# Kernel optimization log

Measured on AMD Instinct MI355X. Metric: run time of the kernel, lower is better.

Reference implementation:

```python
import jax, jax.numpy as jnp
import numpy as np

B, N, IN_DIM, HID = 64, 1024, 128, 32


def _xavier(key, shape):
    # xavier_uniform_ on torch Linear weight [out, in]; we store [in, out]
    fan_in, fan_out = shape[0], shape[1]
    limit = float(np.sqrt(6.0 / (fan_in + fan_out)))
    return jax.random.uniform(key, shape, jnp.float32, -limit, limit)


def setup_inputs() -> dict:
    key = jax.random.key(0)
    ks = jax.random.split(key, 8)
    x = jax.random.normal(ks[0], (B, N, IN_DIM), jnp.float32)
    adj = jax.random.uniform(ks[1], (B, N, N), jnp.float32)  # dense adjacency
    W1 = _xavier(ks[2], (IN_DIM, HID))
    W2 = _xavier(ks[3], (HID, HID))
    W3 = _xavier(ks[4], (HID, HID))
    W4 = _xavier(ks[5], (HID, HID))
    b1 = jnp.zeros((HID,), jnp.float32)
    b2 = jnp.zeros((HID,), jnp.float32)
    b3 = jnp.zeros((HID,), jnp.float32)
    b4 = jnp.zeros((HID,), jnp.float32)
    a1 = jnp.float32(0.25)  # PReLU default init
    a2 = jnp.float32(0.25)
    a3 = jnp.float32(0.25)
    a4 = jnp.float32(0.25)
    return {"x": x, "adj": adj, "W1": W1, "W2": W2, "W3": W3, "W4": W4,
            "b1": b1, "b2": b2, "b3": b3, "b4": b4,
            "a1": a1, "a2": a2, "a3": a3, "a4": a4}


def _gcn_layer(x, adj, W, b, a):
    h = jnp.einsum('bnf,fo->bno', x, W)      # linear, no bias
    h = jnp.matmul(adj, h) + b               # aggregation + bias
    return jnp.where(h >= 0, h, a * h)       # PReLU


def reference(x, adj, W1, W2, W3, W4, b1, b2, b3, b4, a1, a2, a3, a4):
    h1 = _gcn_layer(x, adj, W1, b1, a1)
    h2 = _gcn_layer(h1, adj, W2, b2, a2)
    h3 = _gcn_layer(h2, adj, W3, b3, a3)
    h4 = _gcn_layer(h3, adj, W4, b4, a4)
    # sum-pool nodes per layer, concat along feature dim -> [B, 4*HID]
    return jnp.concatenate([h1.sum(axis=1), h2.sum(axis=1),
                            h3.sum(axis=1), h4.sum(axis=1)], axis=1)
```

## Files before the change

kernel.cpp:

```cpp
#include <hip/hip_runtime.h>
#include <hip/hip_bf16.h>

#define B_   64
#define N_   1024
#define IND_ 128
#define HID_ 32

typedef __attribute__((ext_vector_type(8))) short short8;
typedef __attribute__((ext_vector_type(4))) float f32x4;
typedef unsigned short u16;

static __device__ __forceinline__ u16 f2bf(float f) {
    union { __hip_bfloat16 h; u16 s; } u;
    u.h = __float2bfloat16(f);
    return u.s;
}
static __device__ __forceinline__ short8 cvt8(f32x4 v0, f32x4 v1) {
    union { short8 s; __hip_bfloat162 h[4]; } u;
    u.h[0] = __float22bfloat162_rn(float2{v0[0], v0[1]});
    u.h[1] = __float22bfloat162_rn(float2{v0[2], v0[3]});
    u.h[2] = __float22bfloat162_rn(float2{v1[0], v1[1]});
    u.h[3] = __float22bfloat162_rn(float2{v1[2], v1[3]});
    return u.s;
}

__global__ __launch_bounds__(256) void convert_tile_kernel(
    const float* __restrict__ adjf, u16* __restrict__ adjT)
{
    const int wslot = blockIdx.x * 4 + (threadIdx.x >> 6);
    const int lane = threadIdx.x & 63;
    const int r = lane & 15, g = lane >> 4;
    const int t0 = wslot * 16;
    const int b  = t0 >> 11;
    const int rt = (t0 >> 5) & 63;
    const int k0base = (t0 & 31) * 32;

    const float* src = adjf + ((size_t)b * N_ + rt * 16 + r) * N_ + k0base + g * 8;
    u16* dst = adjT + (size_t)t0 * 512 + lane * 8;
#pragma unroll 4
    for (int j = 0; j < 16; ++j) {
        f32x4 v0 = __builtin_nontemporal_load((const f32x4*)(src + j * 32));
        f32x4 v1 = __builtin_nontemporal_load((const f32x4*)(src + j * 32) + 1);
        *(short8*)(dst + (size_t)j * 512) = cvt8(v0, v1);
    }
}

template<int F>
__global__ __launch_bounds__(256) void linear_kernel(
    const float* __restrict__ in,
    const float* __restrict__ W,
    u16* __restrict__ hF)
{
    __shared__ float sW[F][HID_];
    const int tid = threadIdx.x;
    for (int e = tid; e < F * HID_; e += 256) sW[e / HID_][e % HID_] = W[e];
    __syncthreads();

    const int b = blockIdx.x >> 2;
    const int n = ((blockIdx.x & 3) << 8) + tid;
    const f32x4* row4 = (const f32x4*)(in + ((size_t)b * N_ + n) * F);

    float acc[HID_];
#pragma unroll
    for (int o = 0; o < HID_; ++o) acc[o] = 0.f;

#pragma unroll 4
    for (int f4 = 0; f4 < F / 4; ++f4) {
        f32x4 xv = __builtin_nontemporal_load(row4 + f4);
#pragma unroll
        for (int j = 0; j < 4; ++j)
#pragma unroll
            for (int o = 0; o < HID_; ++o) acc[o] += xv[j] * sW[f4 * 4 + j][o];
    }
    u16* op = hF + (size_t)b * (HID_ * N_) + (size_t)(n >> 5) * 1024
              + ((n >> 3) & 3) * 128 + (n & 7);
#pragma unroll
    for (int o = 0; o < HID_; ++o)
        op[(o >> 4) * 512 + (o & 15) * 8] = f2bf(acc[o]);
}

template<int MODE, int FUSE>
__global__ __launch_bounds__(256) void agg_kernel(
    const float* __restrict__ adjf,
    const u16*  __restrict__ adjT,
    const u16*  __restrict__ hF_in,
    u16*        __restrict__ hF_out,
    const float* __restrict__ Wnext,
    float*      __restrict__ h,
    float*      __restrict__ partial,
    const float* __restrict__ bias,
    const float* __restrict__ alpha_p)
{
    __shared__ float h_s[64][33];
    __shared__ float sW2[HID_][HID_];
    __shared__ float pool[4][HID_];

    const int tid = threadIdx.x;
    const int b = blockIdx.y;
    const int wid = tid >> 6, lane = tid & 63;
    const int r16 = lane & 15, g = lane >> 4;
    const int koff = g * 8;
    const int rowbase = blockIdx.x * 64 + wid * 16;
    const int row0 = rowbase + r16;

    if (FUSE) {
        for (int e = tid; e < HID_ * HID_; e += 256) ((float*)sW2)[e] = Wnext[e];
    }

    const u16* pbF = hF_in + (size_t)b * (HID_ * N_) + lane * 8;
    const u16* pa = (MODE == 0)
        ? adjT + ((size_t)b * 2048 + (size_t)(blockIdx.x * 4 + wid) * 32) * 512 + lane * 8
        : nullptr;
    const float* pf = (MODE == 2)
        ? adjf + ((size_t)b * N_ + row0) * N_ + koff
        : nullptr;

    f32x4 acc[2] = {};
#pragma unroll 8
    for (int ki = 0; ki < 32; ++ki) {
        short8 a0;
        if (MODE == 0) {
            a0 = *(const short8*)(pa + (size_t)ki * 512);
        } else {
            f32x4 v0 = __builtin_nontemporal_load((const f32x4*)(pf + ki * 32));
            f32x4 v1 = __builtin_nontemporal_load((const f32x4*)(pf + ki * 32) + 1);
            a0 = cvt8(v0, v1);
        }
        short8 b0 = *(const short8*)(pbF + (size_t)ki * 1024);
        short8 b1 = *(const short8*)(pbF + (size_t)ki * 1024 + 512);
        acc[0] = __builtin_amdgcn_mfma_f32_16x16x32_bf16(a0, b0, acc[0], 0, 0, 0);
        acc[1] = __builtin_amdgcn_mfma_f32_16x16x32_bf16(a0, b1, acc[1], 0, 0, 0);
    }

    const float alpha = *alpha_p;
    float v[2][4], ps[2];
#pragma unroll
    for (int ct = 0; ct < 2; ++ct) {
        const float bv = bias[ct * 16 + r16];
        ps[ct] = 0.f;
#pragma unroll
        for (int r = 0; r < 4; ++r) {
            float x = acc[ct][r] + bv;
            x = (x >= 0.f) ? x : alpha * x;
            v[ct][r] = x;
            ps[ct] += x;
        }
    }
#pragma unroll
    for (int ct = 0; ct < 2; ++ct) {
        const int col = ct * 16 + r16;
        float p = ps[ct];
        p += __shfl_xor(p, 16, 64);
        p += __shfl_xor(p, 32, 64);
        if (lane < 16) pool[wid][col] = p;
        if (FUSE) {
#pragma unroll
            for (int r = 0; r < 4; ++r)
                h_s[wid * 16 + g * 4 + r][col] = v[ct][r];
        }
        if (MODE == 2) {
#pragma unroll
            for (int r = 0; r < 4; ++r)
                h[((size_t)b * N_ + rowbase + g * 4 + r) * HID_ + col] = v[ct][r];
        }
    }
    __syncthreads();

    if (tid < HID_) {
        float s = pool[0][tid] + pool[1][tid] + pool[2][tid] + pool[3][tid];
        partial[((size_t)b * 16 + blockIdx.x) * HID_ + tid] = s;
    }

    if (FUSE) {
        const int r_local = tid >> 2;
        const int obase = (tid & 3) * 8;
        float acc2[8];
#pragma unroll
        for (int o = 0; o < 8; ++o) acc2[o] = 0.f;
#pragma unroll 4
        for (int k = 0; k < HID_; ++k) {
            const float hv = h_s[r_local][k];
#pragma unroll
            for (int o = 0; o < 8; ++o) acc2[o] += hv * sW2[k][obase + o];
        }
        const int n = blockIdx.x * 64 + r_local;
        u16* op = hF_out + (size_t)b * (HID_ * N_) + (size_t)(n >> 5) * 1024
                  + ((n >> 3) & 3) * 128 + (n & 7);
#pragma unroll
        for (int o = 0; o < 8; ++o) {
            const int oo = obase + o;
            op[(oo >> 4) * 512 + (oo & 15) * 8] = f2bf(acc2[o]);
        }
    }
}

__global__ __launch_bounds__(256) void finalize_kernel(
    const float* __restrict__ partial,
    float* __restrict__ out)
{
    const int i = blockIdx.x * 256 + threadIdx.x;
    if (i >= B_ * 4 * HID_) return;
    const int b = i >> 7;
    const int rem = i & 127;
    const int l = rem >> 5;
    const int o = rem & 31;
    const float* p = partial + (((size_t)l * B_ + b) * 16) * HID_ + o;
    float s = 0.f;
#pragma unroll
    for (int t = 0; t < 16; ++t) s += p[t * HID_];
    out[i] = s;
}

extern "C" void kernel_launch(void* const* d_in, const int* in_sizes, int n_in,
                              void* d_out, int out_size, void* d_ws, size_t ws_size,
                              hipStream_t stream) {
    const float* x   = (const float*)d_in[0];
    const float* adj = (const float*)d_in[1];
    const float* W[4]  = {(const float*)d_in[2], (const float*)d_in[3],
                          (const float*)d_in[4], (const float*)d_in[5]};
    const float* bi[4] = {(const float*)d_in[6], (const float*)d_in[7],
                          (const float*)d_in[8], (const float*)d_in[9]};
    const float* al[4] = {(const float*)d_in[10], (const float*)d_in[11],
                          (const float*)d_in[12], (const float*)d_in[13]};
    float* out = (float*)d_out;

    const size_t adjb_bytes = (size_t)B_ * N_ * N_ * 2;
    const size_t hlin_bytes = (size_t)B_ * HID_ * N_ * 2;
    const size_t h_bytes    = (size_t)B_ * N_ * HID_ * 4;
    const size_t part_bytes = (size_t)4 * B_ * 16 * HID_ * 4;
    const bool full = ws_size >= adjb_bytes + 2 * hlin_bytes + part_bytes;

    const dim3 ga(16, 64);
    const int part_stride = B_ * 16 * HID_;

    if (full) {
        char* p = (char*)d_ws;
        u16* adjT  = (u16*)p;  p += adjb_bytes;
        u16* hFA   = (u16*)p;  p += hlin_bytes;
        u16* hFB   = (u16*)p;  p += hlin_bytes;
        float* partial = (float*)p;

        convert_tile_kernel<<<2048, 256, 0, stream>>>(adj, adjT);
        linear_kernel<IND_><<<256, 256, 0, stream>>>(x, W[0], hFA);

        agg_kernel<0, 1><<<ga, 256, 0, stream>>>(nullptr, adjT, hFA, hFB,
                                                 W[1], nullptr,
                                                 partial + 0, bi[0], al[0]);
        agg_kernel<0, 1><<<ga, 256, 0, stream>>>(nullptr, adjT, hFB, hFA,
                                                 W[2], nullptr,
                                                 partial + (size_t)1 * part_stride,
                                                 bi[1], al[1]);
        agg_kernel<0, 1><<<ga, 256, 0, stream>>>(nullptr, adjT, hFA, hFB,
                                                 W[3], nullptr,
                                                 partial + (size_t)2 * part_stride,
                                                 bi[2], al[2]);
        agg_kernel<0, 0><<<ga, 256, 0, stream>>>(nullptr, adjT, hFB, nullptr,
                                                 nullptr, nullptr,
                                                 partial + (size_t)3 * part_stride,
                                                 bi[3], al[3]);
        finalize_kernel<<<32, 256, 0, stream>>>(partial, out);
    } else {
        char* p = (char*)d_ws;
        u16*   hF      = (u16*)p;  p += hlin_bytes;
        float* h       = (float*)p; p += h_bytes;
        float* partial = (float*)p;

        linear_kernel<IND_><<<256, 256, 0, stream>>>(x, W[0], hF);
        agg_kernel<2, 0><<<ga, 256, 0, stream>>>(adj, nullptr, hF, nullptr,
                                                 nullptr, h, partial, bi[0], al[0]);
        for (int l = 1; l < 4; ++l) {
            linear_kernel<HID_><<<256, 256, 0, stream>>>(h, W[l], hF);
            agg_kernel<2, 0><<<ga, 256, 0, stream>>>(adj, nullptr, hF, nullptr,
                                                     nullptr, h,
                                                     partial + (size_t)l * part_stride,
                                                     bi[l], al[l]);
        }
        finalize_kernel<<<32, 256, 0, stream>>>(partial, out);
    }
}
```

Before: 209.5 us.

## Fuse adjacency bf16 conversion into first aggregation and split K across waves

```diff
diff --git a/kernel.cpp b/kernel.cpp
--- a/kernel.cpp
+++ b/kernel.cpp
@@ -22,27 +22,6 @@
     u.h[2] = __float22bfloat162_rn(float2{v1[0], v1[1]});
     u.h[3] = __float22bfloat162_rn(float2{v1[2], v1[3]});
     return u.s;
-}
-
-__global__ __launch_bounds__(256) void convert_tile_kernel(
-    const float* __restrict__ adjf, u16* __restrict__ adjT)
-{
-    const int wslot = blockIdx.x * 4 + (threadIdx.x >> 6);
-    const int lane = threadIdx.x & 63;
-    const int r = lane & 15, g = lane >> 4;
-    const int t0 = wslot * 16;
-    const int b  = t0 >> 11;
-    const int rt = (t0 >> 5) & 63;
-    const int k0base = (t0 & 31) * 32;
-
-    const float* src = adjf + ((size_t)b * N_ + rt * 16 + r) * N_ + k0base + g * 8;
-    u16* dst = adjT + (size_t)t0 * 512 + lane * 8;
-#pragma unroll 4
-    for (int j = 0; j < 16; ++j) {
-        f32x4 v0 = __builtin_nontemporal_load((const f32x4*)(src + j * 32));
-        f32x4 v1 = __builtin_nontemporal_load((const f32x4*)(src + j * 32) + 1);
-        *(short8*)(dst + (size_t)j * 512) = cvt8(v0, v1);
-    }
 }
 
 template<int F>
@@ -80,9 +59,9 @@
 }
 
 template<int MODE, int FUSE>
-__global__ __launch_bounds__(256) void agg_kernel(
+__global__ __launch_bounds__(512, 8) void agg_kernel(
     const float* __restrict__ adjf,
-    const u16*  __restrict__ adjT,
+    u16*        __restrict__ adjT,
     const u16*  __restrict__ hF_in,
     u16*        __restrict__ hF_out,
     const float* __restrict__ Wnext,
@@ -91,103 +70,120 @@
     const float* __restrict__ bias,
     const float* __restrict__ alpha_p)
 {
+    __shared__ float accx[4][64][8];
     __shared__ float h_s[64][33];
     __shared__ float sW2[HID_][HID_];
     __shared__ float pool[4][HID_];
 
     const int tid = threadIdx.x;
-    const int b = blockIdx.y;
+    const int b = blockIdx.y, bx = blockIdx.x;
     const int wid = tid >> 6, lane = tid & 63;
+    const int kh = wid >> 2, wt = wid & 3;
     const int r16 = lane & 15, g = lane >> 4;
-    const int koff = g * 8;
-    const int rowbase = blockIdx.x * 64 + wid * 16;
-    const int row0 = rowbase + r16;
+    const int rowbase = bx * 64 + wt * 16;
 
     if (FUSE) {
-        for (int e = tid; e < HID_ * HID_; e += 256) ((float*)sW2)[e] = Wnext[e];
-    }
-
-    const u16* pbF = hF_in + (size_t)b * (HID_ * N_) + lane * 8;
-    const u16* pa = (MODE == 0)
-        ? adjT + ((size_t)b * 2048 + (size_t)(blockIdx.x * 4 + wid) * 32) * 512 + lane * 8
-        : nullptr;
-    const float* pf = (MODE == 2)
-        ? adjf + ((size_t)b * N_ + row0) * N_ + koff
-        : nullptr;
+        for (int e = tid; e < HID_ * HID_; e += 512) ((float*)sW2)[e] = Wnext[e];
+    }
+
+    const u16* pbF = hF_in + (size_t)b * (HID_ * N_) + (size_t)kh * 16 * 1024 + lane * 8;
 
     f32x4 acc[2] = {};
+    if (MODE == 0) {
+        const u16* pa = adjT +
+            ((size_t)b * 2048 + (size_t)(bx * 4 + wt) * 32 + kh * 16) * 512 + lane * 8;
 #pragma unroll 8
-    for (int ki = 0; ki < 32; ++ki) {
-        short8 a0;
-        if (MODE == 0) {
-            a0 = *(const short8*)(pa + (size_t)ki * 512);
-        } else {
+        for (int ki = 0; ki < 16; ++ki) {
+            short8 a0 = *(const short8*)(pa + (size_t)ki * 512);
+            short8 b0 = *(const short8*)(pbF + (size_t)ki * 1024);
+            short8 b1 = *(const short8*)(pbF + (size_t)ki * 1024 + 512);
+            acc[0] = __builtin_amdgcn_mfma_f32_16x16x32_bf16(a0, b0, acc[0], 0, 0, 0);
+            acc[1] = __builtin_amdgcn_mfma_f32_16x16x32_bf16(a0, b1, acc[1], 0, 0, 0);
+        }
+    } else {
+        const float* pf = adjf + ((size_t)b * N_ + rowbase + r16) * N_ + kh * 512 + g * 8;
+        u16* po = (MODE == 1)
+            ? adjT + ((size_t)b * 2048 + (size_t)(bx * 4 + wt) * 32 + kh * 16) * 512 + lane * 8
+            : nullptr;
+#pragma unroll 4
+        for (int ki = 0; ki < 16; ++ki) {
             f32x4 v0 = __builtin_nontemporal_load((const f32x4*)(pf + ki * 32));
             f32x4 v1 = __builtin_nontemporal_load((const f32x4*)(pf + ki * 32) + 1);
-            a0 = cvt8(v0, v1);
-        }
-        short8 b0 = *(const short8*)(pbF + (size_t)ki * 1024);
-        short8 b1 = *(const short8*)(pbF + (size_t)ki * 1024 + 512);
-        acc[0] = __builtin_amdgcn_mfma_f32_16x16x32_bf16(a0, b0, acc[0], 0, 0, 0);
-        acc[1] = __builtin_amdgcn_mfma_f32_16x16x32_bf16(a0, b1, acc[1], 0, 0, 0);
-    }
-
-    const float alpha = *alpha_p;
-    float v[2][4], ps[2];
-#pragma unroll
-    for (int ct = 0; ct < 2; ++ct) {
-        const float bv = bias[ct * 16 + r16];
-        ps[ct] = 0.f;
-#pragma unroll
-        for (int r = 0; r < 4; ++r) {
-            float x = acc[ct][r] + bv;
-            x = (x >= 0.f) ? x : alpha * x;
-            v[ct][r] = x;
-            ps[ct] += x;
-        }
-    }
-#pragma unroll
-    for (int ct = 0; ct < 2; ++ct) {
-        const int col = ct * 16 + r16;
-        float p = ps[ct];
-        p += __shfl_xor(p, 16, 64);
-        p += __shfl_xor(p, 32, 64);
-        if (lane < 16) pool[wid][col] = p;
-        if (FUSE) {
-#pragma unroll
-            for (int r = 0; r < 4; ++r)
-                h_s[wid * 16 + g * 4 + r][col] = v[ct][r];
-        }
-        if (MODE == 2) {
-#pragma unroll
-            for (int r = 0; r < 4; ++r)
-                h[((size_t)b * N_ + rowbase + g * 4 + r) * HID_ + col] = v[ct][r];
+            short8 a0 = cvt8(v0, v1);
+            if (MODE == 1) *(short8*)(po + (size_t)ki * 512) = a0;
+            short8 b0 = *(const short8*)(pbF + (size_t)ki * 1024);
+            short8 b1 = *(const short8*)(pbF + (size_t)ki * 1024 + 512);
+            acc[0] = __builtin_amdgcn_mfma_f32_16x16x32_bf16(a0, b0, acc[0], 0, 0, 0);
+            acc[1] = __builtin_amdgcn_mfma_f32_16x16x32_bf16(a0, b1, acc[1], 0, 0, 0);
+        }
+    }
+
+    if (kh == 1) {
+#pragma unroll
+        for (int ct = 0; ct < 2; ++ct)
+#pragma unroll
+            for (int r = 0; r < 4; ++r) accx[wt][lane][ct * 4 + r] = acc[ct][r];
+    }
+    __syncthreads();
+
+    if (kh == 0) {
+        const float alpha = *alpha_p;
+        float v[2][4], ps[2];
+#pragma unroll
+        for (int ct = 0; ct < 2; ++ct) {
+            const float bv = bias[ct * 16 + r16];
+            ps[ct] = 0.f;
+#pragma unroll
+            for (int r = 0; r < 4; ++r) {
+                float x = acc[ct][r] + accx[wt][lane][ct * 4 + r] + bv;
+                x = (x >= 0.f) ? x : alpha * x;
+                v[ct][r] = x;
+                ps[ct] += x;
+            }
+        }
+#pragma unroll
+        for (int ct = 0; ct < 2; ++ct) {
+            const int col = ct * 16 + r16;
+            float p = ps[ct];
+            p += __shfl_xor(p, 16, 64);
+            p += __shfl_xor(p, 32, 64);
+            if (lane < 16) pool[wt][col] = p;
+            if (FUSE) {
+#pragma unroll
+                for (int r = 0; r < 4; ++r)
+                    h_s[wt * 16 + g * 4 + r][col] = v[ct][r];
+            }
+            if (MODE == 2) {
+#pragma unroll
+                for (int r = 0; r < 4; ++r)
+                    h[((size_t)b * N_ + rowbase + g * 4 + r) * HID_ + col] = v[ct][r];
+            }
         }
     }
     __syncthreads();
 
     if (tid < HID_) {
         float s = pool[0][tid] + pool[1][tid] + pool[2][tid] + pool[3][tid];
-        partial[((size_t)b * 16 + blockIdx.x) * HID_ + tid] = s;
+        partial[((size_t)b * 16 + bx) * HID_ + tid] = s;
     }
 
     if (FUSE) {
-        const int r_local = tid >> 2;
-        const int obase = (tid & 3) * 8;
-        float acc2[8];
-#pragma unroll
-        for (int o = 0; o < 8; ++o) acc2[o] = 0.f;
+        const int r_local = tid >> 3;
+        const int obase = (tid & 7) * 4;
+        float acc2[4];
+#pragma unroll
+        for (int o = 0; o < 4; ++o) acc2[o] = 0.f;
 #pragma unroll 4
         for (int k = 0; k < HID_; ++k) {
             const float hv = h_s[r_local][k];
 #pragma unroll
-            for (int o = 0; o < 8; ++o) acc2[o] += hv * sW2[k][obase + o];
-        }
-        const int n = blockIdx.x * 64 + r_local;
+            for (int o = 0; o < 4; ++o) acc2[o] += hv * sW2[k][obase + o];
+        }
+        const int n = bx * 64 + r_local;
         u16* op = hF_out + (size_t)b * (HID_ * N_) + (size_t)(n >> 5) * 1024
                   + ((n >> 3) & 3) * 128 + (n & 7);
 #pragma unroll
-        for (int o = 0; o < 8; ++o) {
+        for (int o = 0; o < 4; ++o) {
             const int oo = obase + o;
             op[(oo >> 4) * 512 + (oo & 15) * 8] = f2bf(acc2[o]);
         }
@@ -240,21 +236,19 @@
         u16* hFB   = (u16*)p;  p += hlin_bytes;
         float* partial = (float*)p;
 
-        convert_tile_kernel<<<2048, 256, 0, stream>>>(adj, adjT);
         linear_kernel<IND_><<<256, 256, 0, stream>>>(x, W[0], hFA);
-
-        agg_kernel<0, 1><<<ga, 256, 0, stream>>>(nullptr, adjT, hFA, hFB,
+        agg_kernel<1, 1><<<ga, 512, 0, stream>>>(adj, adjT, hFA, hFB,
                                                  W[1], nullptr,
                                                  partial + 0, bi[0], al[0]);
-        agg_kernel<0, 1><<<ga, 256, 0, stream>>>(nullptr, adjT, hFB, hFA,
+        agg_kernel<0, 1><<<ga, 512, 0, stream>>>(nullptr, adjT, hFB, hFA,
                                                  W[2], nullptr,
                                                  partial + (size_t)1 * part_stride,
                                                  bi[1], al[1]);
-        agg_kernel<0, 1><<<ga, 256, 0, stream>>>(nullptr, adjT, hFA, hFB,
+        agg_kernel<0, 1><<<ga, 512, 0, stream>>>(nullptr, adjT, hFA, hFB,
                                                  W[3], nullptr,
                                                  partial + (size_t)2 * part_stride,
                                                  bi[2], al[2]);
-        agg_kernel<0, 0><<<ga, 256, 0, stream>>>(nullptr, adjT, hFB, nullptr,
+        agg_kernel<0, 0><<<ga, 512, 0, stream>>>(nullptr, adjT, hFB, nullptr,
                                                  nullptr, nullptr,
                                                  partial + (size_t)3 * part_stride,
                                                  bi[3], al[3]);
@@ -266,11 +260,11 @@
         float* partial = (float*)p;
 
         linear_kernel<IND_><<<256, 256, 0, stream>>>(x, W[0], hF);
-        agg_kernel<2, 0><<<ga, 256, 0, stream>>>(adj, nullptr, hF, nullptr,
+        agg_kernel<2, 0><<<ga, 512, 0, stream>>>(adj, nullptr, hF, nullptr,
                                                  nullptr, h, partial, bi[0], al[0]);
         for (int l = 1; l < 4; ++l) {
             linear_kernel<HID_><<<256, 256, 0, stream>>>(h, W[l], hF);
-            agg_kernel<2, 0><<<ga, 256, 0, stream>>>(adj, nullptr, hF, nullptr,
+            agg_kernel<2, 0><<<ga, 512, 0, stream>>>(adj, nullptr, hF, nullptr,
                                                      nullptr, h,
                                                      partial + (size_t)l * part_stride,
                                                      bi[l], al[l]);
```

Result: faster. 199.4 us (-4.8%).
